# Kernel optimization log

Measured on AMD Instinct MI355X. Metric: run time of the kernel, lower is better.

The kernel has to match this reference:

```python
import jax, jax.numpy as jnp
import numpy as np

D_MODEL = 1024
NUM_HEADS = 16
D_K = D_MODEL // NUM_HEADS
THETA = 10000.0


def setup_inputs() -> dict:
    key = jax.random.key(0)
    ks = jax.random.split(key, 5)
    x = jax.random.normal(ks[0], (4, 2048, D_MODEL), dtype=jnp.float32)
    init = 0.02
    Wq = jax.random.normal(ks[1], (D_MODEL, D_MODEL), dtype=jnp.float32) * init
    Wk = jax.random.normal(ks[2], (D_MODEL, D_MODEL), dtype=jnp.float32) * init
    Wv = jax.random.normal(ks[3], (D_MODEL, D_MODEL), dtype=jnp.float32) * init
    Wo = jax.random.normal(ks[4], (D_MODEL, D_MODEL), dtype=jnp.float32) * init
    return {"x": x, "Wq": Wq, "Wk": Wk, "Wv": Wv, "Wo": Wo}


def _rope(t, positions):
    # t: [B, H, S, d_k]; positions: [S]
    half = D_K // 2
    inv_freq = 1.0 / (THETA ** (jnp.arange(half, dtype=jnp.float32) * 2.0 / D_K))
    ang = positions[:, None].astype(jnp.float32) * inv_freq[None, :]  # [S, half]
    cos, sin = jnp.cos(ang), jnp.sin(ang)
    te = t[..., 0::2]  # even dims [B,H,S,half]
    to = t[..., 1::2]  # odd dims
    re = te * cos - to * sin
    ro = te * sin + to * cos
    # interleave back: [..., half, 2] -> [..., d_k]
    return jnp.stack([re, ro], axis=-1).reshape(t.shape)


def reference(x, Wq, Wk, Wv, Wo):
    B, S, _ = x.shape
    positions = jnp.arange(S)

    def split_heads(t):
        return t.reshape(B, S, NUM_HEADS, D_K).transpose(0, 2, 1, 3)  # [B,H,S,d_k]

    # Linear layers: y = x @ W.T (torch nn.Linear convention, weight [out,in])
    Q = split_heads(x @ Wq.T)
    K = split_heads(x @ Wk.T)
    V = split_heads(x @ Wv.T)

    Q = _rope(Q, positions)
    K = _rope(K, positions)

    scale = 1.0 / jnp.sqrt(jnp.asarray(D_K, dtype=x.dtype))
    scores = jnp.einsum('bhqd,bhkd->bhqk', Q, K) * scale  # [B,H,S,S]
    causal = jnp.tril(jnp.ones((S, S), dtype=bool))
    scores = jnp.where(causal[None, None], scores, jnp.asarray(-jnp.inf, dtype=scores.dtype))
    attn = jax.nn.softmax(scores, axis=-1)
    ctx = jnp.einsum('bhqk,bhkd->bhqd', attn, V)  # [B,H,S,d_k]
    concat = ctx.transpose(0, 2, 1, 3).reshape(B, S, D_MODEL)
    return concat @ Wo.T
```

## Files before the change

kernel.cpp:

```cpp
#include <hip/hip_runtime.h>
#include <hip/hip_bf16.h>

#define BATCH 4
#define SEQ   2048
#define DM    1024
#define NH    16
#define DK    64
#define BH    (BATCH*NH)

typedef __attribute__((ext_vector_type(8))) short  bv8;
typedef __attribute__((ext_vector_type(4))) short  sv4;
typedef __attribute__((ext_vector_type(4))) float  f32x4;

__device__ __forceinline__ short f2b(float f) {
    unsigned u = __builtin_bit_cast(unsigned, f);
    u += 0x7fffu + ((u >> 16) & 1u);
    return (short)(u >> 16);
}
__device__ __forceinline__ unsigned pk2(float lo, float hi) {
    float2 f; f.x = lo; f.y = hi;
    __hip_bfloat162 h = __float22bfloat162_rn(f);
    unsigned r;
    __builtin_memcpy(&r, &h, 4);
    return r;
}
__device__ __forceinline__ float b2f(short s) {
    unsigned u = ((unsigned)(unsigned short)s) << 16;
    return __builtin_bit_cast(float, u);
}

__device__ __forceinline__ void load_lds16(const short* g, short* l) {
    __builtin_amdgcn_global_load_lds(
        (const __attribute__((address_space(1))) void*)g,
        (__attribute__((address_space(3))) void*)l, 16, 0, 0);
}

__global__ __launch_bounds__(256) void cvt_kernel(
    const float* __restrict__ x,
    const float* __restrict__ wq, const float* __restrict__ wk,
    const float* __restrict__ wv, const float* __restrict__ wo,
    short* __restrict__ Xb, short* __restrict__ Wb)
{
    const int f = blockIdx.x;
    const float* src; short* dst; int idx0;
    if (f < 4096) { src = x; dst = Xb; idx0 = f; }
    else {
        int z   = (f - 4096) >> 9;
        int rel = (f - 4096) & 511;
        src = (z == 0) ? wq : (z == 1) ? wk : (z == 2) ? wv : wo;
        dst = Wb + (size_t)z * (DM * DM);
        idx0 = rel;
    }
    int idx = idx0 * 256 + threadIdx.x;
    const float4* s4 = (const float4*)src + (size_t)idx * 2;
    float4 a = s4[0], b = s4[1];
    union { unsigned u[4]; bv8 v; } o;
    o.u[0] = pk2(a.x, a.y);  o.u[1] = pk2(a.z, a.w);
    o.u[2] = pk2(b.x, b.y);  o.u[3] = pk2(b.z, b.w);
    *(bv8*)(dst + (size_t)idx * 8) = o.v;
}

template<bool FINAL>
__global__ __launch_bounds__(256) void gemm_nt(
    const short* __restrict__ A, const short* __restrict__ Wall,
    short* __restrict__ Oq, short* __restrict__ Ok, short* __restrict__ Ov,
    float* __restrict__ FO)
{
    constexpr int K = 1024;
    __shared__ __align__(16) short As[128 * 64];
    __shared__ __align__(16) short Ws[128 * 64];

    const int flat  = (int)blockIdx.x + 8 * (int)blockIdx.y + 512 * (int)blockIdx.z;
    const int chunk = (512 * (int)gridDim.z) >> 3;
    const int L  = (flat & 7) * chunk + (flat >> 3);
    const int bn = L & 7, bm = (L >> 3) & 63, bz = L >> 9;

    const short* Ap; const short* Wp; int row0, col0;
    if (!FINAL && bz == 2) {
        Ap = Wall + 2 * (size_t)(DM * DM);
        Wp = A;
        row0 = bn * 128; col0 = bm * 128;
    } else {
        Ap = A;
        Wp = Wall + (size_t)bz * (DM * DM);
        row0 = bm * 128; col0 = bn * 128;
    }

    const int tid = threadIdx.x;
    const int wave = tid >> 6, lane = tid & 63, lm = lane & 15, lq = lane >> 4;
    const int wr = wave >> 1, wc = wave & 1;

    f32x4 acc[4][4];
    for (int i = 0; i < 4; i++)
        for (int j = 0; j < 4; j++)
            acc[i][j] = f32x4{0.f, 0.f, 0.f, 0.f};

    const int rI = lane >> 3;
    const int cS = (lane & 7) ^ rI;
    const short* gA[4]; const short* gW[4];
    short* lA[4]; short* lW[4];
    for (int j = 0; j < 4; j++) {
        int rl = wave * 32 + j * 8;
        gA[j] = Ap + (size_t)(row0 + rl + rI) * K + cS * 8;
        gW[j] = Wp + (size_t)(col0 + rl + rI) * K + cS * 8;
        lA[j] = &As[rl * 64];
        lW[j] = &Ws[rl * 64];
    }

    for (int kk = 0; kk < K; kk += 64) {
        for (int j = 0; j < 4; j++) {
            load_lds16(gA[j], lA[j]);  gA[j] += 64;
            load_lds16(gW[j], lW[j]);  gW[j] += 64;
        }
        __syncthreads();

        for (int h = 0; h < 2; h++) {
            bv8 af[4], bf[4];
            for (int mt = 0; mt < 4; mt++) {
                int r = wr * 64 + mt * 16 + lm;
                af[mt] = *(const bv8*)&As[r * 64 + (((h * 4 + lq) ^ (lm & 7)) * 8)];
            }
            for (int nt = 0; nt < 4; nt++) {
                int r = wc * 64 + nt * 16 + lm;
                bf[nt] = *(const bv8*)&Ws[r * 64 + (((h * 4 + lq) ^ (lm & 7)) * 8)];
            }
            for (int mt = 0; mt < 4; mt++)
                for (int nt = 0; nt < 4; nt++)
                    acc[mt][nt] = __builtin_amdgcn_mfma_f32_16x16x32_bf16(af[mt], bf[nt], acc[mt][nt], 0, 0, 0);
        }
        __syncthreads();
    }

    if constexpr (FINAL) {
        for (int mt = 0; mt < 4; mt++) {
            int mbase = row0 + wr * 64 + mt * 16 + lq * 4;
            for (int nt = 0; nt < 4; nt++) {
                int n = col0 + wc * 64 + nt * 16 + lm;
                for (int r = 0; r < 4; r++)
                    FO[(size_t)(mbase + r) * DM + n] = acc[mt][nt][r];
            }
        }
    } else if (bz == 2) {
        for (int mt = 0; mt < 4; mt++) {
            int mbase = row0 + wr * 64 + mt * 16 + lq * 4;
            for (int nt = 0; nt < 4; nt++) {
                int n = col0 + wc * 64 + nt * 16 + lm;
                for (int r = 0; r < 4; r++) {
                    int row = mbase + r;
                    int hh = row >> 6, d = row & 63;
                    int b = n >> 11, s = n & 2047;
                    Ov[((size_t)((b * NH + hh) * DK + d)) * SEQ + s] = f2b(acc[mt][nt][r]);
                }
            }
        }
    } else {
        const float scale = (bz == 0) ? 0.125f * 1.44269504089f : 1.0f;
        short* dst = (bz == 0) ? Oq : Ok;
        for (int nt = 0; nt < 4; nt++) {
            int n = col0 + wc * 64 + nt * 16 + lm;
            int h = n >> 6, d = n & 63;
            float invrev = __builtin_amdgcn_exp2f((float)(d >> 1) * -0.41522499f)
                           * 0.15915494309f;
            float sgn = (d & 1) ? 1.0f : -1.0f;
            float swr = __builtin_amdgcn_sinf(invrev);
            float cwr = __builtin_amdgcn_cosf(invrev);
            for (int mt = 0; mt < 4; mt++) {
                int mbase = row0 + wr * 64 + mt * 16 + lq * 4;
                int b = mbase >> 11, s0 = mbase & 2047;
                float rev = __builtin_amdgcn_fractf((float)s0 * invrev);
                float sn = __builtin_amdgcn_sinf(rev);
                float cs = __builtin_amdgcn_cosf(rev);
                size_t obase = ((size_t)((b * NH + h) * SEQ + s0)) * DK + d;
                for (int r = 0; r < 4; r++) {
                    float v  = acc[mt][nt][r];
                    float pv = __shfl_xor(v, 1, 64);
                    float out = (v * cs + sgn * (pv * sn)) * scale;
                    dst[obase + (size_t)r * DK] = f2b(out);
                    float sn2 = sn * cwr + cs * swr;
                    float cs2 = cs * cwr - sn * swr;
                    sn = sn2; cs = cs2;
                }
            }
        }
    }
}

__global__ __launch_bounds__(256, 4) void attn_kernel(
    const short* __restrict__ Qb, const short* __restrict__ Kb,
    const short* __restrict__ Vb, short* __restrict__ Cb)
{
    __shared__ __align__(16) short Ks[2][4096];
    __shared__ __align__(16) short Vs[2][4096];

    const int bx = (int)blockIdx.x;
    const int bh = (int)blockIdx.y;

    const int tid = threadIdx.x, wave = tid >> 6, lane = tid & 63;
    const int lm = lane & 15, lq = lane >> 4;
    const size_t base = (size_t)bh * SEQ * DK;

    const int sr = lane >> 3;
    const int sc = (lane & 7) ^ sr;
    const short* gK0 = Kb + base + (size_t)(wave * 16 + sr) * DK + sc * 8;
    const short* gK1 = Kb + base + (size_t)(wave * 16 + 8 + sr) * DK + sc * 8;
    const short* gV0 = Vb + base + (size_t)(wave * 16 + sr) * SEQ + sc * 8;
    const short* gV1 = Vb + base + (size_t)(wave * 16 + 8 + sr) * SEQ + sc * 8;
    short* lK0[2] = { &Ks[0][(wave * 16) * 64],     &Ks[1][(wave * 16) * 64] };
    short* lK1[2] = { &Ks[0][(wave * 16 + 8) * 64], &Ks[1][(wave * 16 + 8) * 64] };
    short* lV0[2] = { &Vs[0][(wave * 16) * 64],     &Vs[1][(wave * 16) * 64] };
    short* lV1[2] = { &Vs[0][(wave * 16 + 8) * 64], &Vs[1][(wave * 16 + 8) * 64] };

    const int sw = lm & 7;
    const int bb = bh >> 4, hh = bh & 15;
    constexpr int NQT = SEQ / 128;

    for (int pass = 0; pass < 2; ++pass) {
        const int qt = pass ? bx : (NQT - 1 - bx);
        const int q0 = qt * 128;

        bv8 aQ[2][2];
        for (int mg = 0; mg < 2; mg++) {
            const short* qp = Qb + base + (size_t)(q0 + wave * 32 + mg * 16 + lm) * DK + lq * 8;
            aQ[mg][0] = *(const bv8*)qp;
            aQ[mg][1] = *(const bv8*)(qp + 32);
        }

        f32x4 oacc[2][4];
        float rsum[2] = {0.f, 0.f};
        for (int mg = 0; mg < 2; mg++)
            for (int nt = 0; nt < 4; nt++) oacc[mg][nt] = f32x4{0.f, 0.f, 0.f, 0.f};

        const int last = 2 * qt + 1;
        const int qrow_base = q0 + wave * 32 + lm;

        load_lds16(gK0, lK0[0]);  load_lds16(gK1, lK1[0]);
        load_lds16(gV0, lV0[0]);  load_lds16(gV1, lV1[0]);
        __syncthreads();

        for (int kt = 0; kt <= last; ++kt) {
            const int b = kt & 1;
            if (kt < last) {
                const size_t ko = (size_t)(kt + 1) * 64 * DK;
                const size_t vo = (size_t)(kt + 1) * 64;
                load_lds16(gK0 + ko, lK0[b ^ 1]);  load_lds16(gK1 + ko, lK1[b ^ 1]);
                load_lds16(gV0 + vo, lV0[b ^ 1]);  load_lds16(gV1 + vo, lV1[b ^ 1]);
            }

            f32x4 t[2][4];
            for (int nt = 0; nt < 4; nt++) {
                const short* kp = &Ks[b][(nt * 16 + lm) * 64];
                bv8 kf0 = *(const bv8*)(kp + ((lq ^ sw) * 8));
                bv8 kf1 = *(const bv8*)(kp + (((4 + lq) ^ sw) * 8));
                for (int mg = 0; mg < 2; mg++) {
                    f32x4 z = f32x4{0.f, 0.f, 0.f, 0.f};
                    z = __builtin_amdgcn_mfma_f32_16x16x32_bf16(kf0, aQ[mg][0], z, 0, 0, 0);
                    z = __builtin_amdgcn_mfma_f32_16x16x32_bf16(kf1, aQ[mg][1], z, 0, 0, 0);
                    t[mg][nt] = z;
                }
            }

            bv8 aP[2][2];
            for (int mg = 0; mg < 2; mg++) {
                const int qrow = qrow_base + mg * 16;
                if (kt >= 2 * qt) {
                    for (int nt = 0; nt < 4; nt++) {
                        int keyb = kt * 64 + nt * 16 + lq * 4;
                        for (int r = 0; r < 4; r++)
                            t[mg][nt][r] = (keyb + r <= qrow) ? t[mg][nt][r] : -1e30f;
                    }
                }
                for (int nt = 0; nt < 4; nt++)
                    for (int r = 0; r < 4; r++) {
                        float p = __builtin_amdgcn_exp2f(t[mg][nt][r]);
                        rsum[mg] += p;
                        t[mg][nt][r] = p;
                    }
                for (int h = 0; h < 2; h++) {
                    union { unsigned u[4]; bv8 v; } pk;
                    pk.u[0] = pk2(t[mg][2 * h][0],     t[mg][2 * h][1]);
                    pk.u[1] = pk2(t[mg][2 * h][2],     t[mg][2 * h][3]);
                    pk.u[2] = pk2(t[mg][2 * h + 1][0], t[mg][2 * h + 1][1]);
                    pk.u[3] = pk2(t[mg][2 * h + 1][2], t[mg][2 * h + 1][3]);
                    aP[mg][h] = pk.v;
                }
            }

            for (int nt = 0; nt < 4; nt++) {
                const short* vrow = &Vs[b][(nt * 16 + lm) * 64];
                for (int h = 0; h < 2; h++) {
                    int c8 = h * 4 + (lq >> 1);
                    union { sv4 q[2]; bv8 v; } vv;
                    vv.q[0] = *(const sv4*)(vrow + ((c8 ^ sw) * 8)       + (lq & 1) * 4);
                    vv.q[1] = *(const sv4*)(vrow + (((c8 ^ 2) ^ sw) * 8) + (lq & 1) * 4);
                    for (int mg = 0; mg < 2; mg++)
                        oacc[mg][nt] = __builtin_amdgcn_mfma_f32_16x16x32_bf16(aP[mg][h], vv.v, oacc[mg][nt], 0, 0, 0);
                }
            }
            __syncthreads();
        }

        for (int mg = 0; mg < 2; mg++) {
            rsum[mg] += __shfl_xor(rsum[mg], 16, 64);
            rsum[mg] += __shfl_xor(rsum[mg], 32, 64);
        }

        for (int mg = 0; mg < 2; mg++)
            for (int r = 0; r < 4; r++) {
                float l = __shfl(rsum[mg], lq * 4 + r, 64);
                float inv = 1.0f / l;
                int srow = q0 + wave * 32 + mg * 16 + lq * 4 + r;
                size_t rowbase = ((size_t)(bb * SEQ + srow)) * DM + hh * DK;
                for (int nt = 0; nt < 4; nt++)
                    Cb[rowbase + nt * 16 + lm] = f2b(oacc[mg][nt][r] * inv);
            }
    }
}

extern "C" void kernel_launch(void* const* d_in, const int* in_sizes, int n_in,
                              void* d_out, int out_size, void* d_ws, size_t ws_size,
                              hipStream_t stream)
{
    const float* x  = (const float*)d_in[0];
    const float* Wq = (const float*)d_in[1];
    const float* Wk = (const float*)d_in[2];
    const float* Wv = (const float*)d_in[3];
    const float* Wo = (const float*)d_in[4];
    float* out = (float*)d_out;

    const size_t TSZ = (size_t)BH * SEQ * DK;
    short* Qb  = (short*)d_ws;
    short* Kb  = Qb + TSZ;
    short* Vb  = Kb + TSZ;
    short* XCb = Vb + TSZ;
    short* Wb  = XCb + TSZ;

    cvt_kernel<<<dim3(6144), 256, 0, stream>>>(x, Wq, Wk, Wv, Wo, XCb, Wb);
    gemm_nt<false><<<dim3(8, 64, 3), 256, 0, stream>>>(
        XCb, Wb, Qb, Kb, Vb, nullptr);
    attn_kernel<<<dim3(SEQ / 256, BH), 256, 0, stream>>>(Qb, Kb, Vb, XCb);
    gemm_nt<true><<<dim3(8, 64, 1), 256, 0, stream>>>(
        XCb, Wb + 3 * (size_t)(DM * DM), nullptr, nullptr, nullptr, out);
}
```

Baseline: 237.0 us.

## Triple-buffer K/V tiles in attention with partial vmcnt waits

The attention loop now keeps three LDS buffers for K and V and prefetches two tiles ahead instead of one. The per-iteration __syncthreads is replaced by an explicit s_waitcnt vmcnt(4) plus s_barrier, so the newest tile's loads can remain in flight while the current tile is consumed. LDS use grows from 32KB to 48KB per block, which may reduce occupancy at launch bounds of 4 blocks per CU. The vmcnt count must match the number of outstanding load instructions exactly.

```diff
diff --git a/kernel.cpp b/kernel.cpp
--- a/kernel.cpp
+++ b/kernel.cpp
@@ -189,8 +189,8 @@
     const short* __restrict__ Qb, const short* __restrict__ Kb,
     const short* __restrict__ Vb, short* __restrict__ Cb)
 {
-    __shared__ __align__(16) short Ks[2][4096];
-    __shared__ __align__(16) short Vs[2][4096];
+    __shared__ __align__(16) short Ks[3][4096];
+    __shared__ __align__(16) short Vs[3][4096];
 
     const int bx = (int)blockIdx.x;
     const int bh = (int)blockIdx.y;
@@ -205,10 +205,10 @@
     const short* gK1 = Kb + base + (size_t)(wave * 16 + 8 + sr) * DK + sc * 8;
     const short* gV0 = Vb + base + (size_t)(wave * 16 + sr) * SEQ + sc * 8;
     const short* gV1 = Vb + base + (size_t)(wave * 16 + 8 + sr) * SEQ + sc * 8;
-    short* lK0[2] = { &Ks[0][(wave * 16) * 64],     &Ks[1][(wave * 16) * 64] };
-    short* lK1[2] = { &Ks[0][(wave * 16 + 8) * 64], &Ks[1][(wave * 16 + 8) * 64] };
-    short* lV0[2] = { &Vs[0][(wave * 16) * 64],     &Vs[1][(wave * 16) * 64] };
-    short* lV1[2] = { &Vs[0][(wave * 16 + 8) * 64], &Vs[1][(wave * 16 + 8) * 64] };
+    short* lK0[3] = { &Ks[0][(wave * 16) * 64],     &Ks[1][(wave * 16) * 64],     &Ks[2][(wave * 16) * 64] };
+    short* lK1[3] = { &Ks[0][(wave * 16 + 8) * 64], &Ks[1][(wave * 16 + 8) * 64], &Ks[2][(wave * 16 + 8) * 64] };
+    short* lV0[3] = { &Vs[0][(wave * 16) * 64],     &Vs[1][(wave * 16) * 64],     &Vs[2][(wave * 16) * 64] };
+    short* lV1[3] = { &Vs[0][(wave * 16 + 8) * 64], &Vs[1][(wave * 16 + 8) * 64], &Vs[2][(wave * 16 + 8) * 64] };
 
     const int sw = lm & 7;
     const int bb = bh >> 4, hh = bh & 15;
@@ -233,17 +233,25 @@
         const int last = 2 * qt + 1;
         const int qrow_base = q0 + wave * 32 + lm;
 
-        load_lds16(gK0, lK0[0]);  load_lds16(gK1, lK1[0]);
-        load_lds16(gV0, lV0[0]);  load_lds16(gV1, lV1[0]);
-        __syncthreads();
+        {
+            load_lds16(gK0, lK0[0]);  load_lds16(gK1, lK1[0]);
+            load_lds16(gV0, lV0[0]);  load_lds16(gV1, lV1[0]);
+            const size_t ko = (size_t)64 * DK, vo = 64;
+            load_lds16(gK0 + ko, lK0[1]);  load_lds16(gK1 + ko, lK1[1]);
+            load_lds16(gV0 + vo, lV0[1]);  load_lds16(gV1 + vo, lV1[1]);
+        }
+        asm volatile("s_waitcnt vmcnt(0)" ::: "memory");
+        __builtin_amdgcn_s_barrier();
+        __builtin_amdgcn_sched_barrier(0);
 
         for (int kt = 0; kt <= last; ++kt) {
-            const int b = kt & 1;
-            if (kt < last) {
-                const size_t ko = (size_t)(kt + 1) * 64 * DK;
-                const size_t vo = (size_t)(kt + 1) * 64;
-                load_lds16(gK0 + ko, lK0[b ^ 1]);  load_lds16(gK1 + ko, lK1[b ^ 1]);
-                load_lds16(gV0 + vo, lV0[b ^ 1]);  load_lds16(gV1 + vo, lV1[b ^ 1]);
+            const int b = kt % 3;
+            if (kt + 2 <= last) {
+                const int bn2 = (b == 0) ? 2 : b - 1;
+                const size_t ko = (size_t)(kt + 2) * 64 * DK;
+                const size_t vo = (size_t)(kt + 2) * 64;
+                load_lds16(gK0 + ko, lK0[bn2]);  load_lds16(gK1 + ko, lK1[bn2]);
+                load_lds16(gV0 + vo, lV0[bn2]);  load_lds16(gV1 + vo, lV1[bn2]);
             }
 
             f32x4 t[2][4];
@@ -296,7 +304,15 @@
                         oacc[mg][nt] = __builtin_amdgcn_mfma_f32_16x16x32_bf16(aP[mg][h], vv.v, oacc[mg][nt], 0, 0, 0);
                 }
             }
-            __syncthreads();
+
+            if (kt < last) {
+                if (kt + 2 <= last)
+                    asm volatile("s_waitcnt vmcnt(4)" ::: "memory");
+                else
+                    asm volatile("s_waitcnt vmcnt(0)" ::: "memory");
+                __builtin_amdgcn_s_barrier();
+                __builtin_amdgcn_sched_barrier(0);
+            }
         }
 
         for (int mg = 0; mg < 2; mg++) {
@@ -313,6 +329,8 @@
                 for (int nt = 0; nt < 4; nt++)
                     Cb[rowbase + nt * 16 + lm] = f2b(oacc[mg][nt][r] * inv);
             }
+
+        __syncthreads();
     }
 }
 
```

Measured after the change: 248.3 us. 1.05x slower.

## Enlarge GEMM tiles to 256x128 with 8 waves and triple-buffered LDS pipeline

Applied to the files above, without the earlier changes.

The projection GEMMs now use 512-thread blocks computing 256x128 tiles, with 8 waves each owning a 64x64 sub-tile. Global-to-LDS loads are triple-buffered, using explicit vmcnt waits and a single barrier per k-step, so the next two k-slices load while the current one is computed. This targets exposed load latency and doubled barriers in the previous single-buffer loop and raises reuse of A across more columns. In exchange it needs more LDS per block (about 144 KB), which may cap residency. The epilogue still indexes rows with wr and a 4-wave layout, so correctness depends on code not shown.

```diff
diff --git a/kernel.cpp b/kernel.cpp
--- a/kernel.cpp
+++ b/kernel.cpp
@@ -61,29 +61,40 @@
 }
 
 template<bool FINAL>
-__global__ __launch_bounds__(256) void gemm_nt(
+__global__ __launch_bounds__(512, 2) void gemm8(
     const short* __restrict__ A, const short* __restrict__ Wall,
     short* __restrict__ Oq, short* __restrict__ Ok, short* __restrict__ Ov,
     float* __restrict__ FO)
 {
-    constexpr int K = 1024;
-    __shared__ __align__(16) short As[128 * 64];
-    __shared__ __align__(16) short Ws[128 * 64];
-
-    const int flat  = (int)blockIdx.x + 8 * (int)blockIdx.y + 512 * (int)blockIdx.z;
-    const int chunk = (512 * (int)gridDim.z) >> 3;
-    const int L  = (flat & 7) * chunk + (flat >> 3);
-    const int bn = L & 7, bm = (L >> 3) & 63, bz = L >> 9;
-
-    const short* Ap; const short* Wp; int row0, col0;
-    if (!FINAL && bz == 2) {
-        Ap = Wall + 2 * (size_t)(DM * DM);
-        Wp = A;
-        row0 = bn * 128; col0 = bm * 128;
+    constexpr int K   = 1024;
+    constexpr int NT  = 16;
+    constexpr int ASZ = 256 * 64;
+    constexpr int WSZ = 128 * 64;
+    __shared__ __align__(16) short As[3 * ASZ];
+    __shared__ __align__(16) short Ws[3 * WSZ];
+
+    const int flat = (int)blockIdx.x;
+    int bz = 0, row0, col0;
+    const short* Ap; const short* Wp;
+    if constexpr (!FINAL) {
+        const int L = (flat & 7) * 96 + (flat >> 3);
+        bz = L >> 8;  const int rem = L & 255;
+        if (bz == 2) {
+            Ap = Wall + 2 * (size_t)(DM * DM);
+            Wp = A;
+            row0 = (rem >> 6) * 256;
+            col0 = (rem & 63) * 128;
+        } else {
+            Ap = A;
+            Wp = Wall + (size_t)bz * (DM * DM);
+            row0 = (rem >> 3) * 256;
+            col0 = (rem & 7) * 128;
+        }
     } else {
-        Ap = A;
-        Wp = Wall + (size_t)bz * (DM * DM);
-        row0 = bm * 128; col0 = bn * 128;
+        const int L = (flat & 7) * 32 + (flat >> 3);
+        Ap = A; Wp = Wall;
+        row0 = (L >> 3) * 256;
+        col0 = (L & 7) * 128;
     }
 
     const int tid = threadIdx.x;
@@ -91,44 +102,78 @@
     const int wr = wave >> 1, wc = wave & 1;
 
     f32x4 acc[4][4];
+    #pragma unroll
     for (int i = 0; i < 4; i++)
+        #pragma unroll
         for (int j = 0; j < 4; j++)
             acc[i][j] = f32x4{0.f, 0.f, 0.f, 0.f};
 
     const int rI = lane >> 3;
     const int cS = (lane & 7) ^ rI;
-    const short* gA[4]; const short* gW[4];
-    short* lA[4]; short* lW[4];
+    const short* gA[4]; short* lA[4];
+    #pragma unroll
     for (int j = 0; j < 4; j++) {
         int rl = wave * 32 + j * 8;
         gA[j] = Ap + (size_t)(row0 + rl + rI) * K + cS * 8;
+        lA[j] = &As[rl * 64];
+    }
+    const short* gW[2]; short* lW[2];
+    #pragma unroll
+    for (int j = 0; j < 2; j++) {
+        int rl = wave * 16 + j * 8;
         gW[j] = Wp + (size_t)(col0 + rl + rI) * K + cS * 8;
-        lA[j] = &As[rl * 64];
         lW[j] = &Ws[rl * 64];
     }
 
-    for (int kk = 0; kk < K; kk += 64) {
-        for (int j = 0; j < 4; j++) {
-            load_lds16(gA[j], lA[j]);  gA[j] += 64;
-            load_lds16(gW[j], lW[j]);  gW[j] += 64;
-        }
-        __syncthreads();
-
+    auto stage = [&](int buf) {
+        #pragma unroll
+        for (int j = 0; j < 4; j++) { load_lds16(gA[j], lA[j] + buf * ASZ); gA[j] += 64; }
+        #pragma unroll
+        for (int j = 0; j < 2; j++) { load_lds16(gW[j], lW[j] + buf * WSZ); gW[j] += 64; }
+    };
+    auto compute = [&](int buf) {
+        const short* Ab = &As[buf * ASZ];
+        const short* Wb2 = &Ws[buf * WSZ];
+        #pragma unroll
         for (int h = 0; h < 2; h++) {
             bv8 af[4], bf[4];
+            #pragma unroll
             for (int mt = 0; mt < 4; mt++) {
                 int r = wr * 64 + mt * 16 + lm;
-                af[mt] = *(const bv8*)&As[r * 64 + (((h * 4 + lq) ^ (lm & 7)) * 8)];
-            }
+                af[mt] = *(const bv8*)&Ab[r * 64 + (((h * 4 + lq) ^ (lm & 7)) * 8)];
+            }
+            #pragma unroll
             for (int nt = 0; nt < 4; nt++) {
                 int r = wc * 64 + nt * 16 + lm;
-                bf[nt] = *(const bv8*)&Ws[r * 64 + (((h * 4 + lq) ^ (lm & 7)) * 8)];
-            }
+                bf[nt] = *(const bv8*)&Wb2[r * 64 + (((h * 4 + lq) ^ (lm & 7)) * 8)];
+            }
+            #pragma unroll
             for (int mt = 0; mt < 4; mt++)
+                #pragma unroll
                 for (int nt = 0; nt < 4; nt++)
                     acc[mt][nt] = __builtin_amdgcn_mfma_f32_16x16x32_bf16(af[mt], bf[nt], acc[mt][nt], 0, 0, 0);
         }
-        __syncthreads();
+    };
+
+    stage(0);
+    __builtin_amdgcn_sched_barrier(0);
+    stage(1);
+    asm volatile("s_waitcnt vmcnt(6)" ::: "memory");
+    __builtin_amdgcn_s_barrier();
+    __builtin_amdgcn_sched_barrier(0);
+
+    int cb = 0, sb = 2;
+    for (int t = 0; t < NT; ++t) {
+        if (t < NT - 2) stage(sb);
+        compute(cb);
+        if (t < NT - 1) {
+            if (t < NT - 2) asm volatile("s_waitcnt vmcnt(6)" ::: "memory");
+            else            asm volatile("s_waitcnt vmcnt(0)" ::: "memory");
+            __builtin_amdgcn_s_barrier();
+            __builtin_amdgcn_sched_barrier(0);
+        }
+        cb = (cb == 2) ? 0 : cb + 1;
+        sb = (sb == 2) ? 0 : sb + 1;
     }
 
     if constexpr (FINAL) {
@@ -335,9 +380,9 @@
     short* Wb  = XCb + TSZ;
 
     cvt_kernel<<<dim3(6144), 256, 0, stream>>>(x, Wq, Wk, Wv, Wo, XCb, Wb);
-    gemm_nt<false><<<dim3(8, 64, 3), 256, 0, stream>>>(
+    gemm8<false><<<dim3(768), 512, 0, stream>>>(
         XCb, Wb, Qb, Kb, Vb, nullptr);
     attn_kernel<<<dim3(SEQ / 256, BH), 256, 0, stream>>>(Qb, Kb, Vb, XCb);
-    gemm_nt<true><<<dim3(8, 64, 1), 256, 0, stream>>>(
+    gemm8<true><<<dim3(256), 512, 0, stream>>>(
         XCb, Wb + 3 * (size_t)(DM * DM), nullptr, nullptr, nullptr, out);
 }
```

New measurement: 244.7 us. +3.3%, slower.
